# Kernel tuning notes

Measured on AMD Instinct MI355X. Metric: run time of the kernel, lower is better.

Reference implementation:

```python
import jax, jax.numpy as jnp
import numpy as np
import math

B, T, F_ = 4, 1024, 1024
TO_DIM, FROM_DIM, LATENT, H = 1024, 1024, 1024, 16
HEAD_DIM = LATENT // H

def _linear_params(key, in_dim, out_dim):
    kw, kb = jax.random.split(key)
    bound = 1.0 / math.sqrt(in_dim)
    W = jax.random.uniform(kw, (out_dim, in_dim), minval=-bound, maxval=bound, dtype=jnp.float32)
    b = jax.random.uniform(kb, (out_dim,), minval=-bound, maxval=bound, dtype=jnp.float32)
    return W, b

def setup_inputs() -> dict:
    key = jax.random.key(0)
    ks = jax.random.split(key, 7)
    X_to = jax.random.normal(ks[0], (B, T, TO_DIM), dtype=jnp.float32)
    X_from = jax.random.normal(ks[1], (B, F_, FROM_DIM), dtype=jnp.float32)
    mask_from = jax.random.randint(ks[2], (B, T, F_), 0, 2, dtype=jnp.int32)
    Wq, bq = _linear_params(ks[3], TO_DIM, LATENT)
    Wk, bk = _linear_params(ks[4], FROM_DIM, LATENT)
    Wv, bv = _linear_params(ks[5], FROM_DIM, LATENT)
    Wo, bo = _linear_params(ks[6], LATENT, TO_DIM)
    return {"X_to": X_to, "X_from": X_from, "mask_from": mask_from,
            "Wq": Wq, "bq": bq, "Wk": Wk, "bk": bk, "Wv": Wv, "bv": bv, "Wo": Wo, "bo": bo}

def _split_heads(x):
    # [b, t, (h k)] -> [b, h, t, k]
    b, t, _ = x.shape
    return x.reshape(b, t, H, HEAD_DIM).transpose(0, 2, 1, 3)

def reference(X_to, X_from, mask_from, Wq, bq, Wk, bk, Wv, bv, Wo, bo):
    Q = _split_heads(X_to @ Wq.T + bq)
    # NOTE: source swaps names — K comes from v_linear, V from k_linear. Reproduced literally.
    K = _split_heads(X_from @ Wv.T + bv)
    V = _split_heads(X_from @ Wk.T + bk)
    attn = jnp.einsum('bhtk,bhfk->bhtf', Q, K) / math.sqrt(HEAD_DIM)
    attn = jnp.where(mask_from[:, None, :, :] == 0, jnp.float32(-10000.0), attn)
    attn = jax.nn.softmax(attn, axis=-1)
    out = jnp.einsum('bhtf,bhfk->bhtk', attn, V)  # [b,h,t,k]
    out = out.transpose(0, 2, 1, 3).reshape(X_to.shape[0], X_to.shape[1], LATENT)
    return out @ Wo.T + bo
```

## Files before the change

### kernel.cpp

```cpp
#include <hip/hip_runtime.h>
#include <hip/hip_bf16.h>
#include <math.h>

#define BB 4
#define TT 1024
#define FF 1024
#define DIM 1024
#define NH 16
#define HD 64
#define MROWS (BB * TT)
#define FB (FF / 64)

typedef __attribute__((ext_vector_type(8))) short short8;
typedef __attribute__((ext_vector_type(4))) short short4v;
typedef __attribute__((ext_vector_type(4))) float f32x4;
typedef __hip_bfloat16 bf16;

__device__ __forceinline__ void async_copy16(const void* g, void* l) {
    __builtin_amdgcn_global_load_lds((const __attribute__((address_space(1))) void*)g,
                                     (__attribute__((address_space(3))) void*)l,
                                     16, 0, 0);
}

#define BARRIER() __builtin_amdgcn_s_barrier()

struct ConvArgs {
    const float* src[6];
    bf16* dst[6];
    int nvec[6];
    int blk_end[6];
    const int* mask;
    unsigned long long* Mb;
};

__global__ __launch_bounds__(256) void convert_pack(ConvArgs a) {
    int bx = blockIdx.x;
    if (bx >= a.blk_end[5]) {
        const int lane = threadIdx.x & 63;
        const int waveId = (bx - a.blk_end[5]) * 4 + (threadIdx.x >> 6);
#pragma unroll
        for (int it = 0; it < 16; ++it) {
            int c = waveId * 16 + it;
            int v = a.mask[(size_t)c * 64 + lane];
            unsigned long long bits = __ballot(v != 0);
            if (lane == 0) a.Mb[c] = bits;
        }
        return;
    }
    int seg = 0;
#pragma unroll
    for (int k = 0; k < 5; ++k) if (bx >= a.blk_end[k]) seg = k + 1;
    int b0 = seg ? a.blk_end[seg - 1] : 0;
    int idx = (bx - b0) * 256 + threadIdx.x;
    if (idx >= a.nvec[seg]) return;
    float4 v = ((const float4*)a.src[seg])[idx];
    union { bf16 t[4]; ushort4 u; } o;
    o.t[0] = __float2bfloat16(v.x);
    o.t[1] = __float2bfloat16(v.y);
    o.t[2] = __float2bfloat16(v.z);
    o.t[3] = __float2bfloat16(v.w);
    *(ushort4*)(a.dst[seg] + 4 * (size_t)idx) = o.u;
}

#define BK 64

struct QkvArgs {
    const bf16* A[3]; const bf16* W[3]; const float* bias[3]; bf16* C[3];
    int N[3]; int biasRow[3]; float scale[3];
};

__global__ __launch_bounds__(256, 2) void gemm_qkv(QkvArgs q) {
    __shared__ bf16 lds[32768];

    const int op = blockIdx.z;
    const bf16* A = q.A[op];
    const bf16* W = q.W[op];
    const float* bias = q.bias[op];
    bf16* C = q.C[op];
    const int N = q.N[op];
    const int brow = q.biasRow[op];
    const float sc = q.scale[op];

    const int lin = blockIdx.x + 8 * blockIdx.y;
    const int xcd = lin & 7;
    const int t8  = lin >> 3;
    int m0, n0;
    if (brow) {
        m0 = (((t8 & 7) + xcd) & 7) * 128;
        n0 = (xcd * 4 + (t8 >> 3)) * 128;
    } else {
        m0 = (xcd * 4 + (t8 >> 3)) * 128;
        n0 = (((t8 & 7) + xcd) & 7) * 128;
    }

    const int tid  = threadIdx.x;
    const int lane = tid & 63;
    const int wave = tid >> 6;
    const int quad = lane >> 4;
    const int l16  = lane & 15;
    const int wm = wave & 1;
    const int wn = wave >> 1;
    const int wbase = tid & ~63;

    const int srow = tid >> 3;
    const int scol = (tid & 7) ^ (srow & 7);
    const bf16* pA = A + (size_t)(m0 + srow) * DIM + scol * 8;
    const bf16* pB = W + (size_t)(n0 + srow) * DIM + scol * 8;

#define STAGE(T) do { \
    const bf16* sa_ = pA + (size_t)(T) * 64; \
    const bf16* sb_ = pB + (size_t)(T) * 64; \
    bf16* base_ = lds + ((T) & 1) * 16384; \
    _Pragma("unroll") for (int j = 0; j < 4; ++j) { \
        async_copy16(sa_ + (size_t)(j * 32) * DIM, base_ + (j * 256 + wbase) * 8); \
        async_copy16(sb_ + (size_t)(j * 32) * DIM, base_ + 8192 + (j * 256 + wbase) * 8); \
    } \
} while (0)

    f32x4 acc[4][4] = {};

    STAGE(0); STAGE(1);
    asm volatile("s_waitcnt vmcnt(8)");
    BARRIER();

#pragma unroll 2
    for (int t = 0; t < 16; ++t) {
        const bf16* As = lds + (t & 1) * 16384;
        const bf16* Bs = As + 8192;

        short8 a2[2][4], b2[2][4];
#pragma unroll
        for (int kk = 0; kk < 2; ++kk) {
#pragma unroll
            for (int mi = 0; mi < 4; ++mi) {
                int r = wm * 64 + mi * 16 + l16;
                int p = (kk * 4 + quad) ^ (r & 7);
                a2[kk][mi] = *(const short8*)(As + r * 64 + p * 8);
            }
#pragma unroll
            for (int ni = 0; ni < 4; ++ni) {
                int r = wn * 64 + ni * 16 + l16;
                int p = (kk * 4 + quad) ^ (r & 7);
                b2[kk][ni] = *(const short8*)(Bs + r * 64 + p * 8);
            }
        }
        __builtin_amdgcn_s_setprio(1);
#pragma unroll
        for (int kk = 0; kk < 2; ++kk)
#pragma unroll
            for (int mi = 0; mi < 4; ++mi)
#pragma unroll
                for (int ni = 0; ni < 4; ++ni)
                    acc[mi][ni] = __builtin_amdgcn_mfma_f32_16x16x32_bf16(
                        a2[kk][mi], b2[kk][ni], acc[mi][ni], 0, 0, 0);
        __builtin_amdgcn_s_setprio(0);

        BARRIER();
        if (t + 2 < 16) STAGE(t + 2);
        if (t < 14)       { asm volatile("s_waitcnt vmcnt(8)"); }
        else if (t == 14) { asm volatile("s_waitcnt vmcnt(0)"); }
        BARRIER();
    }

    bf16* Cs = lds;
#pragma unroll
    for (int ni = 0; ni < 4; ++ni) {
        const int nl = wn * 64 + ni * 16 + l16;
        float bcol = brow ? 0.0f : bias[n0 + nl];
#pragma unroll
        for (int mi = 0; mi < 4; ++mi)
#pragma unroll
            for (int i = 0; i < 4; ++i) {
                const int ml = wm * 64 + mi * 16 + quad * 4 + i;
                float v = (acc[mi][ni][i] + (brow ? bias[m0 + ml] : bcol)) * sc;
                Cs[ml * 132 + nl] = __float2bfloat16(v);
            }
    }
    __syncthreads();
#pragma unroll
    for (int j = 0; j < 8; ++j) {
        int slot = j * 256 + tid;
        int rr = slot >> 4, cc = slot & 15;
        short8 v = *(const short8*)(Cs + rr * 132 + cc * 8);
        *(short8*)(C + (size_t)(m0 + rr) * N + n0 + cc * 8) = v;
    }
#undef STAGE
}

__global__ __launch_bounds__(256, 2) void gemm_o(
    const bf16* __restrict__ A, const bf16* __restrict__ W,
    const float* __restrict__ bias, float* __restrict__ C)
{
    __shared__ bf16 lds[24576];

    const int lin = blockIdx.x + 16 * blockIdx.y;
    const int xcd = lin & 7;
    const int t8  = lin >> 3;
    const int m0 = (xcd * 4 + (t8 >> 4)) * 128;
    const int n0 = (((t8 & 15) + 2 * xcd) & 15) * 64;

    const int tid  = threadIdx.x;
    const int lane = tid & 63;
    const int wave = tid >> 6;
    const int quad = lane >> 4;
    const int l16  = lane & 15;
    const int wm = wave & 1;
    const int wn = wave >> 1;
    const int wbase = tid & ~63;

    const int srow = tid >> 3;
    const int scol = (tid & 7) ^ (srow & 7);
    const bf16* pA = A + (size_t)(m0 + srow) * DIM + scol * 8;
    const bf16* pB = W + (size_t)(n0 + srow) * DIM + scol * 8;

#define STAGE_O(T) do { \
    const bf16* sa_ = pA + (size_t)(T) * 64; \
    const bf16* sb_ = pB + (size_t)(T) * 64; \
    bf16* ab_ = lds + ((T) & 1) * 8192; \
    bf16* bb_ = lds + 16384 + ((T) & 1) * 4096; \
    _Pragma("unroll") for (int j = 0; j < 4; ++j) \
        async_copy16(sa_ + (size_t)(j * 32) * DIM, ab_ + (j * 256 + wbase) * 8); \
    _Pragma("unroll") for (int j = 0; j < 2; ++j) \
        async_copy16(sb_ + (size_t)(j * 32) * DIM, bb_ + (j * 256 + wbase) * 8); \
} while (0)

    f32x4 acc[4][2] = {};

    STAGE_O(0); STAGE_O(1);
    asm volatile("s_waitcnt vmcnt(6)");
    BARRIER();

#pragma unroll 2
    for (int t = 0; t < 16; ++t) {
        const bf16* As = lds + (t & 1) * 8192;
        const bf16* Bs = lds + 16384 + (t & 1) * 4096;

        short8 a2[2][4], b2[2][2];
#pragma unroll
        for (int kk = 0; kk < 2; ++kk) {
#pragma unroll
            for (int mi = 0; mi < 4; ++mi) {
                int r = wm * 64 + mi * 16 + l16;
                int p = (kk * 4 + quad) ^ (r & 7);
                a2[kk][mi] = *(const short8*)(As + r * 64 + p * 8);
            }
#pragma unroll
            for (int ni = 0; ni < 2; ++ni) {
                int r = wn * 32 + ni * 16 + l16;
                int p = (kk * 4 + quad) ^ (r & 7);
                b2[kk][ni] = *(const short8*)(Bs + r * 64 + p * 8);
            }
        }
        __builtin_amdgcn_s_setprio(1);
#pragma unroll
        for (int kk = 0; kk < 2; ++kk)
#pragma unroll
            for (int mi = 0; mi < 4; ++mi)
#pragma unroll
                for (int ni = 0; ni < 2; ++ni)
                    acc[mi][ni] = __builtin_amdgcn_mfma_f32_16x16x32_bf16(
                        a2[kk][mi], b2[kk][ni], acc[mi][ni], 0, 0, 0);
        __builtin_amdgcn_s_setprio(0);

        BARRIER();
        if (t + 2 < 16) STAGE_O(t + 2);
        if (t < 14)       { asm volatile("s_waitcnt vmcnt(6)"); }
        else if (t == 14) { asm volatile("s_waitcnt vmcnt(0)"); }
        BARRIER();
    }

    float* Cs = (float*)lds;
#pragma unroll
    for (int ni = 0; ni < 2; ++ni) {
        const int nl = wn * 32 + ni * 16 + l16;
        const float bcol = bias[n0 + nl];
#pragma unroll
        for (int mi = 0; mi < 4; ++mi)
#pragma unroll
            for (int i = 0; i < 4; ++i) {
                const int ml = wm * 64 + mi * 16 + quad * 4 + i;
                Cs[ml * 66 + nl] = acc[mi][ni][i] + bcol;
            }
    }
    __syncthreads();
#pragma unroll
    for (int j = 0; j < 8; ++j) {
        int slot = j * 256 + tid;
        int rr = slot >> 4, cc = slot & 15;
        float4 v = *(const float4*)(Cs + rr * 66 + cc * 4);
        *(float4*)(C + (size_t)(m0 + rr) * DIM + n0 + cc * 4) = v;
    }
#undef STAGE_O
}

__global__ __launch_bounds__(256, 4) void attn_kernel(
    const bf16* Qg, const bf16* __restrict__ Kg, const bf16* __restrict__ Vtg,
    const unsigned long long* __restrict__ Mbits, bf16* Og)
{
    __shared__ bf16 Ks[2 * 64 * 64];
    __shared__ bf16 Vts[2 * 64 * 64];
    __shared__ bf16 Pt[64 * 64];

    const int tid  = threadIdx.x;
    const int lane = tid & 63;
    const int wave = tid >> 6;
    const int quad = lane >> 4;
    const int l16  = lane & 15;

    const int lin = blockIdx.x + 16 * (blockIdx.y + 16 * blockIdx.z);
    const int xcd = lin & 7;
    const int t   = lin >> 3;
    const int bh  = xcd * 8 + (t >> 4);
    const int b   = bh >> 4;
    const int h   = bh & 15;
    const int t0  = (t & 15) * 64;

    const size_t qrow0 = (size_t)b * TT + t0;
    const size_t krow0 = (size_t)b * FF;
    const int wbase = tid & ~63;
    const int myrow = wave * 16 + l16;
    const int pswz  = (l16 & 7) << 4;
    char* ptb = (char*)Pt + myrow * 128;

    const bf16* qptr = Qg + (qrow0 + myrow) * DIM + h * HD;
    short8 qb0 = *(const short8*)(qptr + quad * 8);
    short8 qb1 = *(const short8*)(qptr + 32 + quad * 8);

    const int srow = tid >> 3;
    const int sg   = ((tid & 7) ^ (srow & 7)) * 8;
    const bf16* kS = Kg + (krow0 + srow) * DIM + h * HD + sg;
    const bf16* vS = Vtg + (size_t)(h * HD + srow) * MROWS + b * FF + sg;

#define STAGE_K(SLOT, IT) do { \
    const bf16* ks_ = kS + (size_t)((IT) * 64) * DIM; \
    bf16* kd_ = Ks + (SLOT) * 4096 + wbase * 8; \
    async_copy16(ks_, kd_); \
    async_copy16(ks_ + (size_t)32 * DIM, kd_ + 2048); \
} while (0)

#define STAGE_V(SLOT, IT) do { \
    const bf16* vs_ = vS + (IT) * 64; \
    bf16* vd_ = Vts + (SLOT) * 4096 + wbase * 8; \
    async_copy16(vs_, vd_); \
    async_copy16(vs_ + (size_t)32 * MROWS, vd_ + 2048); \
} while (0)

#define QK_CLUSTER(DST, KPTR) do { \
    _Pragma("unroll") for (int ft = 0; ft < 4; ++ft) { \
        int r_ = ft * 16 + l16; \
        short8 ka0 = *(const short8*)((KPTR) + r_ * 64 + ((quad       ^ (r_ & 7)) * 8)); \
        short8 ka1 = *(const short8*)((KPTR) + r_ * 64 + (((quad + 4) ^ (r_ & 7)) * 8)); \
        f32x4 s_ = {}; \
        s_ = __builtin_amdgcn_mfma_f32_16x16x32_bf16(ka0, qb0, s_, 0, 0, 0); \
        s_ = __builtin_amdgcn_mfma_f32_16x16x32_bf16(ka1, qb1, s_, 0, 0, 0); \
        (DST)[ft] = s_; \
    } \
} while (0)

    const unsigned long long* mrow = Mbits + (qrow0 + myrow) * FB;
    unsigned long long w = mrow[0];

    float lsum = 0.f;
    f32x4 oacc[4] = {};

    STAGE_K(0, 0); STAGE_K(1, 1); STAGE_V(0, 0); STAGE_V(1, 1);
    asm volatile("s_waitcnt vmcnt(2)");
    BARRIER();

    f32x4 scur[4];
    QK_CLUSTER(scur, Ks);
    BARRIER();

#pragma unroll 2
    for (int it = 0; it < 16; ++it) {
        if (it + 2 < 16) STAGE_K((it + 2) & 1, it + 2);

        const bf16* Vc = Vts + (it & 1) * 4096;

        unsigned long long nw = (it < 15) ? mrow[it + 1] : 0;

        f32x4 snxt[4] = {};
        if (it < 15) QK_CLUSTER(snxt, Ks + ((it + 1) & 1) * 4096);

#pragma unroll
        for (int ft = 0; ft < 4; ++ft) {
            const unsigned bits4 =
                (unsigned)(w >> (ft * 16 + quad * 4)) & 0xFu;
            union { short4v v; short s[4]; } pk;
            float psum = 0.f;
#pragma unroll
            for (int i = 0; i < 4; ++i) {
                float p = (bits4 >> i) & 1u ? __expf(scur[ft][i]) : 0.f;
                psum += p;
                pk.s[i] = (short)__bfloat16_as_ushort(__float2bfloat16(p));
            }
            lsum += psum;
            *(short4v*)(ptb + ((ft * 32 + quad * 8) ^ pswz)) = pk.v;
        }
        w = nw;

        short8 pa[2];
        pa[0] = *(const short8*)(ptb + ((quad * 16) ^ pswz));
        pa[1] = *(const short8*)(ptb + ((64 + quad * 16) ^ pswz));
        __builtin_amdgcn_s_setprio(1);
#pragma unroll
        for (int nt = 0; nt < 4; ++nt) {
            int rd = nt * 16 + l16;
#pragma unroll
            for (int kf = 0; kf < 2; ++kf) {
                int g = (kf * 4 + quad) ^ (rd & 7);
                short8 vb = *(const short8*)(Vc + rd * 64 + g * 8);
                oacc[nt] = __builtin_amdgcn_mfma_f32_16x16x32_bf16(pa[kf], vb, oacc[nt], 0, 0, 0);
            }
        }
        __builtin_amdgcn_s_setprio(0);

        BARRIER();
        if (it + 2 < 16) STAGE_V((it + 2) & 1, it + 2);
        if (it < 14)       { asm volatile("s_waitcnt vmcnt(2)"); }
        else if (it == 14) { asm volatile("s_waitcnt vmcnt(0)"); }
        BARRIER();

        scur[0] = snxt[0]; scur[1] = snxt[1];
        scur[2] = snxt[2]; scur[3] = snxt[3];
    }
#undef STAGE_K
#undef STAGE_V
#undef QK_CLUSTER

    lsum += __shfl_xor(lsum, 16);
    lsum += __shfl_xor(lsum, 32);

#pragma unroll
    for (int i = 0; i < 4; ++i) {
        float inv = 1.0f / __shfl(lsum, quad * 4 + i);
        const int prow = wave * 16 + quad * 4 + i;
#pragma unroll
        for (int nt = 0; nt < 4; ++nt)
            Pt[prow * 64 + nt * 16 + l16] = __float2bfloat16(oacc[nt][i] * inv);
    }
    __syncthreads();
#pragma unroll
    for (int j = 0; j < 2; ++j) {
        int s = j * 256 + tid;
        int rr = s >> 3, off = (s & 7) * 8;
        short8 v = *(const short8*)(Pt + rr * 64 + off);
        *(short8*)(Og + (qrow0 + rr) * DIM + h * HD + off) = v;
    }
}

extern "C" void kernel_launch(void* const* d_in, const int* in_sizes, int n_in,
                              void* d_out, int out_size, void* d_ws, size_t ws_size,
                              hipStream_t stream) {
    const float* X_to   = (const float*)d_in[0];
    const float* X_from = (const float*)d_in[1];
    const int*   mask   = (const int*)  d_in[2];
    const float* Wq     = (const float*)d_in[3];
    const float* bq     = (const float*)d_in[4];
    const float* Wk     = (const float*)d_in[5];
    const float* bk     = (const float*)d_in[6];
    const float* Wv     = (const float*)d_in[7];
    const float* bv     = (const float*)d_in[8];
    const float* Wo     = (const float*)d_in[9];
    const float* bo     = (const float*)d_in[10];
    float* out = (float*)d_out;

    char* ws = (char*)d_ws;
    bf16* Xt16 = (bf16*)(ws);
    bf16* Xf16 = (bf16*)(ws + (8u  << 20));
    bf16* Wq16 = (bf16*)(ws + (16u << 20));
    bf16* Wv16 = (bf16*)(ws + (18u << 20));
    bf16* Wk16 = (bf16*)(ws + (20u << 20));
    bf16* Wo16 = (bf16*)(ws + (22u << 20));
    bf16* Q16  = (bf16*)(ws + (24u << 20));
    bf16* K16  = (bf16*)(ws + (32u << 20));
    bf16* Vt16 = (bf16*)(ws + (40u << 20));
    unsigned long long* Mb = (unsigned long long*)(ws + (48u << 20));

    ConvArgs ca;
    ca.src[0] = X_to;   ca.dst[0] = Xt16; ca.nvec[0] = MROWS * DIM / 4;
    ca.src[1] = X_from; ca.dst[1] = Xf16; ca.nvec[1] = MROWS * DIM / 4;
    ca.src[2] = Wq;     ca.dst[2] = Wq16; ca.nvec[2] = DIM * DIM / 4;
    ca.src[3] = Wv;     ca.dst[3] = Wv16; ca.nvec[3] = DIM * DIM / 4;
    ca.src[4] = Wk;     ca.dst[4] = Wk16; ca.nvec[4] = DIM * DIM / 4;
    ca.src[5] = Wo;     ca.dst[5] = Wo16; ca.nvec[5] = DIM * DIM / 4;
    int cum = 0;
    for (int k = 0; k < 6; ++k) { cum += ca.nvec[k] / 256; ca.blk_end[k] = cum; }
    ca.mask = mask; ca.Mb = Mb;
    convert_pack<<<cum + 1024, 256, 0, stream>>>(ca);

    QkvArgs qa;
    qa.A[0] = Xt16; qa.W[0] = Wq16; qa.bias[0] = bq; qa.C[0] = Q16;
    qa.N[0] = DIM; qa.biasRow[0] = 0; qa.scale[0] = 0.125f;
    qa.A[1] = Xf16; qa.W[1] = Wv16; qa.bias[1] = bv; qa.C[1] = K16;
    qa.N[1] = DIM; qa.biasRow[1] = 0; qa.scale[1] = 1.0f;
    qa.A[2] = Wk16; qa.W[2] = Xf16; qa.bias[2] = bk; qa.C[2] = Vt16;
    qa.N[2] = MROWS; qa.biasRow[2] = 1; qa.scale[2] = 1.0f;
    gemm_qkv<<<dim3(8, 32, 3), 256, 0, stream>>>(qa);

    attn_kernel<<<dim3(TT / 64, NH, BB), 256, 0, stream>>>(
        Q16, K16, Vt16, Mb, Q16);

    gemm_o<<<dim3(DIM / 64, MROWS / 128), 256, 0, stream>>>(Q16, Wo16, bo, out);
}
```

Baseline: 205.5 us.

## Load V fragments directly from global into registers, bypassing LDS staging

Drops the double-buffered LDS staging of the transposed V tile. Each wave now loads its V MFMA operands straight from global memory into registers at the top of every iteration, and K prefetch is reordered to reuse the slot freed in the previous iteration. This removes the LDS writes and reads for V and frees LDS space. In exchange, each of the four waves fetches the whole V tile, so global and L2 traffic for V goes up fourfold. The per-iteration full vmcnt(0) wait also reduces how far K and V loads can overlap compute.

```diff
diff --git a/kernel.cpp b/kernel.cpp
--- a/kernel.cpp
+++ b/kernel.cpp
@@ -298,7 +298,6 @@
     const unsigned long long* __restrict__ Mbits, bf16* Og)
 {
     __shared__ bf16 Ks[2 * 64 * 64];
-    __shared__ bf16 Vts[2 * 64 * 64];
     __shared__ bf16 Pt[64 * 64];
 
     const int tid  = threadIdx.x;
@@ -329,20 +328,13 @@
     const int srow = tid >> 3;
     const int sg   = ((tid & 7) ^ (srow & 7)) * 8;
     const bf16* kS = Kg + (krow0 + srow) * DIM + h * HD + sg;
-    const bf16* vS = Vtg + (size_t)(h * HD + srow) * MROWS + b * FF + sg;
+    const bf16* vB = Vtg + (size_t)(h * HD + l16) * MROWS + b * FF + quad * 8;
 
 #define STAGE_K(SLOT, IT) do { \
     const bf16* ks_ = kS + (size_t)((IT) * 64) * DIM; \
     bf16* kd_ = Ks + (SLOT) * 4096 + wbase * 8; \
     async_copy16(ks_, kd_); \
     async_copy16(ks_ + (size_t)32 * DIM, kd_ + 2048); \
-} while (0)
-
-#define STAGE_V(SLOT, IT) do { \
-    const bf16* vs_ = vS + (IT) * 64; \
-    bf16* vd_ = Vts + (SLOT) * 4096 + wbase * 8; \
-    async_copy16(vs_, vd_); \
-    async_copy16(vs_ + (size_t)32 * MROWS, vd_ + 2048); \
 } while (0)
 
 #define QK_CLUSTER(DST, KPTR) do { \
@@ -363,8 +355,8 @@
     float lsum = 0.f;
     f32x4 oacc[4] = {};
 
-    STAGE_K(0, 0); STAGE_K(1, 1); STAGE_V(0, 0); STAGE_V(1, 1);
-    asm volatile("s_waitcnt vmcnt(2)");
+    STAGE_K(0, 0); STAGE_K(1, 1);
+    asm volatile("s_waitcnt vmcnt(0)");
     BARRIER();
 
     f32x4 scur[4];
@@ -373,9 +365,16 @@
 
 #pragma unroll 2
     for (int it = 0; it < 16; ++it) {
-        if (it + 2 < 16) STAGE_K((it + 2) & 1, it + 2);
-
-        const bf16* Vc = Vts + (it & 1) * 4096;
+        short8 vbr[8];
+        const bf16* vb_ = vB + it * 64;
+#pragma unroll
+        for (int nt = 0; nt < 4; ++nt)
+#pragma unroll
+            for (int kf = 0; kf < 2; ++kf)
+                vbr[nt * 2 + kf] =
+                    *(const short8*)(vb_ + (size_t)(nt * 16) * MROWS + kf * 32);
+
+        if (it + 2 < 16) STAGE_K(it & 1, it + 2);
 
         unsigned long long nw = (it < 15) ? mrow[it + 1] : 0;
 
@@ -404,28 +403,21 @@
         pa[1] = *(const short8*)(ptb + ((64 + quad * 16) ^ pswz));
         __builtin_amdgcn_s_setprio(1);
 #pragma unroll
-        for (int nt = 0; nt < 4; ++nt) {
-            int rd = nt * 16 + l16;
-#pragma unroll
-            for (int kf = 0; kf < 2; ++kf) {
-                int g = (kf * 4 + quad) ^ (rd & 7);
-                short8 vb = *(const short8*)(Vc + rd * 64 + g * 8);
-                oacc[nt] = __builtin_amdgcn_mfma_f32_16x16x32_bf16(pa[kf], vb, oacc[nt], 0, 0, 0);
-            }
-        }
+        for (int nt = 0; nt < 4; ++nt)
+#pragma unroll
+            for (int kf = 0; kf < 2; ++kf)
+                oacc[nt] = __builtin_amdgcn_mfma_f32_16x16x32_bf16(
+                    pa[kf], vbr[nt * 2 + kf], oacc[nt], 0, 0, 0);
         __builtin_amdgcn_s_setprio(0);
 
         BARRIER();
-        if (it + 2 < 16) STAGE_V((it + 2) & 1, it + 2);
-        if (it < 14)       { asm volatile("s_waitcnt vmcnt(2)"); }
-        else if (it == 14) { asm volatile("s_waitcnt vmcnt(0)"); }
+        asm volatile("s_waitcnt vmcnt(0)");
         BARRIER();
 
         scur[0] = snxt[0]; scur[1] = snxt[1];
         scur[2] = snxt[2]; scur[3] = snxt[3];
     }
 #undef STAGE_K
-#undef STAGE_V
 #undef QK_CLUSTER
 
     lsum += __shfl_xor(lsum, 16);
```

Result: slower. 255.4 us (+24.3%).
